# Kernel optimization log

Measured on AMD Instinct MI355X. Metric: run time of the kernel, lower is better.

## Reference

```python
import jax, jax.numpy as jnp
import numpy as np

N = 100_000      # nodes
E = 1_600_000    # directed edges (avg degree 16)
DIN, DH, DOUT = 128, 256, 40
BN_EPS = 1e-5


def setup_inputs() -> dict:
    key = jax.random.key(0)
    ks = jax.random.split(key, 8)
    x = jax.random.normal(ks[0], (N, DIN), jnp.float32)
    edge_index = jax.random.randint(ks[1], (2, E), 0, N, dtype=jnp.int64)
    W0 = jax.random.normal(ks[2], (DIN, DH), jnp.float32) / np.float32(np.sqrt(DIN))
    b0 = jnp.zeros((DH,), jnp.float32)
    Wh = jax.random.normal(ks[3], (3, DH, DH), jnp.float32) / np.float32(np.sqrt(DH))
    bh = jnp.zeros((3, DH), jnp.float32)
    gamma = jnp.ones((4, DH), jnp.float32)
    beta = jnp.zeros((4, DH), jnp.float32)
    Wl = jax.random.normal(ks[4], (DH, DOUT), jnp.float32) / np.float32(np.sqrt(DH))
    bl = jnp.zeros((DOUT,), jnp.float32)
    return dict(x=x, W0=W0, b0=b0, Wh=Wh, bh=bh, gamma=gamma, beta=beta,
                Wl=Wl, bl=bl, edge_index=edge_index)


def _gcn_conv(x, W, b, row, col, norm):
    # x: [N, Din] -> [N, Dout]; GCNConv: D^-1/2 (A+I) D^-1/2 (X W) + b
    h = x @ W
    msg = h[col] * norm[:, None]          # gather over edges [E+N, Dout]
    agg = jax.ops.segment_sum(msg, row, num_segments=N)
    return agg + b


def _bn(x, g, b):
    # BatchNorm1d training-mode math: batch stats over nodes, biased variance
    mu = x.mean(axis=0)
    var = x.var(axis=0)
    return (x - mu) * jax.lax.rsqrt(var + BN_EPS) * g + b


def reference(x, W0, b0, Wh, bh, gamma, beta, Wl, bl, edge_index):
    loop = jnp.arange(N, dtype=edge_index.dtype)
    row = jnp.concatenate([edge_index[0], loop])   # add self-loops
    col = jnp.concatenate([edge_index[1], loop])
    deg = jax.ops.segment_sum(jnp.ones_like(row, x.dtype), row, num_segments=N)
    dinv = jnp.where(deg > 0, jax.lax.rsqrt(jnp.maximum(deg, 1e-12)), 0.0)
    norm = dinv[row] * dinv[col]

    h = _gcn_conv(x, W0, b0, row, col, norm)
    h = jax.nn.relu(_bn(h, gamma[0], beta[0]))
    for i in range(3):
        h = _gcn_conv(h, Wh[i], bh[i], row, col, norm)
        h = jax.nn.relu(_bn(h, gamma[i + 1], beta[i + 1]))
    h = _gcn_conv(h, Wl, bl, row, col, norm)
    return jax.nn.log_softmax(h, axis=-1)
```

## Files before the change

kernel.cpp:

```cpp
#include <hip/hip_runtime.h>
#include <hip/hip_bf16.h>
#include <math.h>
#include <stdint.h>

#define N_NODES 100000
#define N_EDGES 1600000
#define DIN 128
#define DH 256
#define DOUT 40
#define DOUTP 48
#define BN_EPS 1e-5f
#define SCAN_BLOCKS ((N_NODES + 1023) / 1024)

#define RPB 512
#define NBKT ((N_NODES + RPB - 1) / RPB)
#define BCAP 10240
#define EPB 8192

#define AGG_GRID 2048

typedef __attribute__((ext_vector_type(8))) short short8;
typedef __attribute__((ext_vector_type(4))) short short4v;
typedef __attribute__((ext_vector_type(4))) float floatx4;

__device__ __forceinline__ short f2bf(float f) {
    uint32_t u = __float_as_uint(f);
    uint32_t r = u + 0x7FFF + ((u >> 16) & 1);
    return (short)(r >> 16);
}
__device__ __forceinline__ float bf_lo(uint32_t u) { return __uint_as_float(u << 16); }
__device__ __forceinline__ float bf_hi(uint32_t u) { return __uint_as_float(u & 0xFFFF0000u); }
__device__ __forceinline__ float bfval(short s) {
    return __uint_as_float(((uint32_t)(unsigned short)s) << 16);
}


__global__ __launch_bounds__(256) void k_bucket(
    const int* __restrict__ row, const int* __restrict__ col,
    int* __restrict__ cnt, int* __restrict__ bcnt, int2* __restrict__ bkt) {
    __shared__ int lcnt[NBKT];
    __shared__ int gbase[NBKT];
    __shared__ unsigned short parr[EPB];
    const int t = threadIdx.x;
    const int e0 = blockIdx.x * EPB;
    for (int i = t; i < NBKT; i += 256) lcnt[i] = 0;
    __syncthreads();
    for (int i = t; i < EPB; i += 256) {
        int e = e0 + i;
        if (e < N_EDGES) {
            int r = row[e];
            atomicAdd(&cnt[r], 1);
            int b = r >> 9;
            parr[i] = (unsigned short)atomicAdd(&lcnt[b], 1);
        }
    }
    __syncthreads();
    for (int i = t; i < NBKT; i += 256)
        gbase[i] = atomicAdd(&bcnt[i], lcnt[i]);
    __syncthreads();
    for (int i = t; i < EPB; i += 256) {
        int e = e0 + i;
        if (e < N_EDGES) {
            int r = row[e];
            int c = col[e];
            int b = r >> 9;
            int pos = gbase[b] + (int)parr[i];
            if (pos < BCAP) bkt[(size_t)b * BCAP + pos] = make_int2(r, c);
        }
    }
}

__global__ __launch_bounds__(256) void k_scan_a(const int* __restrict__ cnt,
                                                int* __restrict__ rowptr,
                                                int* __restrict__ partials,
                                                float* __restrict__ dinv, int n) {
    int t = threadIdx.x;
    int idx = blockIdx.x * 1024 + t * 4;
    int a0 = 0, a1 = 0, a2 = 0, a3 = 0;
    if (idx + 3 < n) {
        int4 v = *(const int4*)(cnt + idx);
        a0 = v.x + 1; a1 = v.y + 1; a2 = v.z + 1; a3 = v.w + 1;
    } else {
        if (idx + 0 < n) a0 = cnt[idx + 0] + 1;
        if (idx + 1 < n) a1 = cnt[idx + 1] + 1;
        if (idx + 2 < n) a2 = cnt[idx + 2] + 1;
        if (idx + 3 < n) a3 = cnt[idx + 3] + 1;
    }
    if (idx + 0 < n) dinv[idx + 0] = rsqrtf((float)a0);
    if (idx + 1 < n) dinv[idx + 1] = rsqrtf((float)a1);
    if (idx + 2 < n) dinv[idx + 2] = rsqrtf((float)a2);
    if (idx + 3 < n) dinv[idx + 3] = rsqrtf((float)a3);
    int tsum = a0 + a1 + a2 + a3;
    int lane = t & 63, wid = t >> 6;
    int incl = tsum;
#pragma unroll
    for (int off = 1; off < 64; off <<= 1) {
        int x = __shfl_up(incl, off);
        if (lane >= off) incl += x;
    }
    __shared__ int wsum[4];
    if (lane == 63) wsum[wid] = incl;
    __syncthreads();
    int woff = 0;
    for (int i = 0; i < wid; i++) woff += wsum[i];
    int excl = woff + incl - tsum;
    if (idx + 0 < n) rowptr[idx + 0] = excl;
    if (idx + 1 < n) rowptr[idx + 1] = excl + a0;
    if (idx + 2 < n) rowptr[idx + 2] = excl + a0 + a1;
    if (idx + 3 < n) rowptr[idx + 3] = excl + a0 + a1 + a2;
    if (t == 255) partials[blockIdx.x] = woff + incl;
}

__global__ __launch_bounds__(128) void k_scan_b(int* __restrict__ partials,
                                                int* __restrict__ rowptr,
                                                int nb, int n) {
    int t = threadIdx.x;
    int v = (t < nb) ? partials[t] : 0;
    int lane = t & 63, wid = t >> 6;
    int incl = v;
#pragma unroll
    for (int off = 1; off < 64; off <<= 1) {
        int x = __shfl_up(incl, off);
        if (lane >= off) incl += x;
    }
    __shared__ int ws[2];
    if (lane == 63) ws[wid] = incl;
    __syncthreads();
    int woff = (wid == 1) ? ws[0] : 0;
    int excl = woff + incl - v;
    if (t < nb) partials[t] = excl;
    if (t == nb - 1) rowptr[n] = excl + v;
}

__global__ __launch_bounds__(256) void k_scan_c(int* __restrict__ rowptr,
                                                const int* __restrict__ partials, int n) {
    int off = partials[blockIdx.x];
    if (off == 0) return;
    int idx = blockIdx.x * 1024 + threadIdx.x * 4;
    if (idx + 3 < n) {
        int4 v = *(const int4*)(rowptr + idx);
        v.x += off; v.y += off; v.z += off; v.w += off;
        *(int4*)(rowptr + idx) = v;
    } else {
        for (int i = 0; i < 4; i++)
            if (idx + i < n) rowptr[idx + i] += off;
    }
}

__global__ __launch_bounds__(256) void k_fillcsr(
    const int* __restrict__ bcnt, const int2* __restrict__ bkt,
    const int* __restrict__ rowptr, int* __restrict__ colidx) {
    __shared__ int lfill[RPB];
    const int b = blockIdx.x, t = threadIdx.x;
    const int base_row = b * RPB;
    for (int i = t; i < RPB; i += 256) lfill[i] = 0;
    __syncthreads();
    int n = bcnt[b]; if (n > BCAP) n = BCAP;
    const int2* bp = bkt + (size_t)b * BCAP;
    for (int i = t; i < n; i += 256) {
        int2 rc = bp[i];
        int p = atomicAdd(&lfill[rc.x - base_row], 1);
        colidx[rowptr[rc.x] + p] = rc.y;
    }
    __syncthreads();
    for (int i = t; i < RPB; i += 256) {
        int r = base_row + i;
        if (r < N_NODES) colidx[rowptr[r + 1] - 1] = r;
    }
}


__global__ void k_prep_all(const float* __restrict__ W0, const float* __restrict__ Wh,
                           const float* __restrict__ Wl, short* __restrict__ wt0,
                           short* __restrict__ wth, short* __restrict__ wtl) {
    int idx = blockIdx.x * blockDim.x + threadIdx.x;
    if (idx < DH * DIN) {
        int n = idx / DIN, k = idx - n * DIN;
        wt0[idx] = f2bf(W0[(size_t)k * DH + n]);
        return;
    }
    idx -= DH * DIN;
    if (idx < 3 * DH * DH) {
        int m = idx / (DH * DH);
        int r = idx - m * (DH * DH);
        int n = r / DH, k = r - n * DH;
        wth[idx] = f2bf(Wh[(size_t)m * DH * DH + (size_t)k * DH + n]);
        return;
    }
    idx -= 3 * DH * DH;
    if (idx < DOUTP * DH) {
        int n = idx / DH, k = idx - n * DH;
        wtl[idx] = (n < DOUT) ? f2bf(Wl[(size_t)k * DOUT + n]) : (short)0;
    }
}


#define BM 64
#define BN_T 256
#define BK 64
#define BKP 72

template <bool ABF16, bool BN_ACT>
__global__ __launch_bounds__(256) void k_gemm_mfma(
    const void* __restrict__ Ap, const short* __restrict__ Wt,
    short* __restrict__ Chs, const float* __restrict__ dinv,
    const float* __restrict__ scale, const float* __restrict__ shift,
    int M, int K) {
    __shared__ __align__(16) short Als[BM * BKP];
    __shared__ __align__(16) short Bls[BN_T * BKP];
    const int t = threadIdx.x;
    const int bm = blockIdx.x * BM;
    const int w = t >> 6, lane = t & 63;
    const int wm = w & 1, wn = w >> 1;
    const int l15 = lane & 15, quad = lane >> 4;

    floatx4 acc[2][8] = {};

    for (int k0 = 0; k0 < K; k0 += BK) {
        {
            int r = t >> 2;
            int c = t & 3;
            int gr = bm + r; if (gr >= M) gr = M - 1;
            short* lp = Als + r * BKP + c * 16;
            if (ABF16) {
                const short* ap = (const short*)Ap + (size_t)gr * K + k0 + c * 16;
                short8 s0 = *(const short8*)(ap);
                short8 s1 = *(const short8*)(ap + 8);
                if (BN_ACT) {
#pragma unroll
                    for (int i = 0; i < 2; i++) {
                        float4 sc = *(const float4*)(scale + k0 + c * 16 + i * 8);
                        float4 sc2 = *(const float4*)(scale + k0 + c * 16 + i * 8 + 4);
                        float4 sh = *(const float4*)(shift + k0 + c * 16 + i * 8);
                        float4 sh2 = *(const float4*)(shift + k0 + c * 16 + i * 8 + 4);
                        short8& s = i ? s1 : s0;
                        short8 o;
                        o[0] = f2bf(fmaxf(fmaf(bfval(s[0]), sc.x, sh.x), 0.f));
                        o[1] = f2bf(fmaxf(fmaf(bfval(s[1]), sc.y, sh.y), 0.f));
                        o[2] = f2bf(fmaxf(fmaf(bfval(s[2]), sc.z, sh.z), 0.f));
                        o[3] = f2bf(fmaxf(fmaf(bfval(s[3]), sc.w, sh.w), 0.f));
                        o[4] = f2bf(fmaxf(fmaf(bfval(s[4]), sc2.x, sh2.x), 0.f));
                        o[5] = f2bf(fmaxf(fmaf(bfval(s[5]), sc2.y, sh2.y), 0.f));
                        o[6] = f2bf(fmaxf(fmaf(bfval(s[6]), sc2.z, sh2.z), 0.f));
                        o[7] = f2bf(fmaxf(fmaf(bfval(s[7]), sc2.w, sh2.w), 0.f));
                        *(short8*)(lp + i * 8) = o;
                    }
                } else {
                    *(short8*)(lp) = s0;
                    *(short8*)(lp + 8) = s1;
                }
            } else {
                const float* ap = (const float*)Ap + (size_t)gr * K + k0 + c * 16;
#pragma unroll
                for (int i = 0; i < 4; i++) {
                    float4 v = *(const float4*)(ap + i * 4);
                    short4v s;
                    s.x = f2bf(v.x); s.y = f2bf(v.y); s.z = f2bf(v.z); s.w = f2bf(v.w);
                    *(short4v*)(lp + i * 4) = s;
                }
            }
        }
        {
            int r0 = t >> 2;
            int c = t & 3;
#pragma unroll
            for (int p = 0; p < 4; p++) {
                int r = r0 + p * 64;
                const short* bp = Wt + (size_t)r * K + k0 + c * 16;
                short* lp = Bls + r * BKP + c * 16;
                *(short8*)(lp) = *(const short8*)(bp);
                *(short8*)(lp + 8) = *(const short8*)(bp + 8);
            }
        }
        __syncthreads();
#pragma unroll
        for (int kc = 0; kc < 2; kc++) {
            short8 af[2], bfr[8];
#pragma unroll
            for (int mi = 0; mi < 2; mi++)
                af[mi] = *(const short8*)(Als + (wm * 32 + mi * 16 + l15) * BKP + kc * 32 + quad * 8);
#pragma unroll
            for (int ni = 0; ni < 8; ni++)
                bfr[ni] = *(const short8*)(Bls + (wn * 128 + ni * 16 + l15) * BKP + kc * 32 + quad * 8);
#pragma unroll
            for (int mi = 0; mi < 2; mi++)
#pragma unroll
                for (int ni = 0; ni < 8; ni++)
                    acc[mi][ni] = __builtin_amdgcn_mfma_f32_16x16x32_bf16(
                        af[mi], bfr[ni], acc[mi][ni], 0, 0, 0);
        }
        __syncthreads();
    }

#pragma unroll
    for (int mi = 0; mi < 2; mi++) {
#pragma unroll
        for (int r = 0; r < 4; r++) {
            int m = bm + wm * 32 + mi * 16 + quad * 4 + r;
            if (m < M) {
                float d = dinv[m];
                size_t base = (size_t)m * BN_T + wn * 128 + l15;
#pragma unroll
                for (int ni = 0; ni < 8; ni++)
                    Chs[base + ni * 16] = f2bf(acc[mi][ni][r] * d);
            }
        }
    }
}


__global__ __launch_bounds__(256) void k_gemm_last(
    const short* __restrict__ A, const short* __restrict__ Wt,
    short* __restrict__ C, const float* __restrict__ dinv,
    const float* __restrict__ scale, const float* __restrict__ shift, int M) {
    __shared__ __align__(16) short Als[BM * BKP];
    __shared__ __align__(16) short Bls[DOUTP * BKP];
    const int t = threadIdx.x;
    const int bm = blockIdx.x * BM;
    const int w = t >> 6, lane = t & 63;
    const int l15 = lane & 15, quad = lane >> 4;
    const int K = DH;

    floatx4 acc[3] = {};

    for (int k0 = 0; k0 < K; k0 += BK) {
        {
            int r = t >> 2;
            int c = t & 3;
            int gr = bm + r; if (gr >= M) gr = M - 1;
            const short* ap = A + (size_t)gr * K + k0 + c * 16;
            short* lp = Als + r * BKP + c * 16;
            short8 s0 = *(const short8*)(ap);
            short8 s1 = *(const short8*)(ap + 8);
#pragma unroll
            for (int i = 0; i < 2; i++) {
                float4 sc = *(const float4*)(scale + k0 + c * 16 + i * 8);
                float4 sc2 = *(const float4*)(scale + k0 + c * 16 + i * 8 + 4);
                float4 sh = *(const float4*)(shift + k0 + c * 16 + i * 8);
                float4 sh2 = *(const float4*)(shift + k0 + c * 16 + i * 8 + 4);
                short8& s = i ? s1 : s0;
                short8 o;
                o[0] = f2bf(fmaxf(fmaf(bfval(s[0]), sc.x, sh.x), 0.f));
                o[1] = f2bf(fmaxf(fmaf(bfval(s[1]), sc.y, sh.y), 0.f));
                o[2] = f2bf(fmaxf(fmaf(bfval(s[2]), sc.z, sh.z), 0.f));
                o[3] = f2bf(fmaxf(fmaf(bfval(s[3]), sc.w, sh.w), 0.f));
                o[4] = f2bf(fmaxf(fmaf(bfval(s[4]), sc2.x, sh2.x), 0.f));
                o[5] = f2bf(fmaxf(fmaf(bfval(s[5]), sc2.y, sh2.y), 0.f));
                o[6] = f2bf(fmaxf(fmaf(bfval(s[6]), sc2.z, sh2.z), 0.f));
                o[7] = f2bf(fmaxf(fmaf(bfval(s[7]), sc2.w, sh2.w), 0.f));
                *(short8*)(lp + i * 8) = o;
            }
        }
        if (t < 192) {
            int r = t >> 2;
            int c = t & 3;
            const short* bp = Wt + (size_t)r * K + k0 + c * 16;
            short* lp = Bls + r * BKP + c * 16;
            *(short8*)(lp) = *(const short8*)(bp);
            *(short8*)(lp + 8) = *(const short8*)(bp + 8);
        }
        __syncthreads();
#pragma unroll
        for (int kc = 0; kc < 2; kc++) {
            short8 af = *(const short8*)(Als + (w * 16 + l15) * BKP + kc * 32 + quad * 8);
#pragma unroll
            for (int ni = 0; ni < 3; ni++) {
                short8 bfr = *(const short8*)(Bls + (ni * 16 + l15) * BKP + kc * 32 + quad * 8);
                acc[ni] = __builtin_amdgcn_mfma_f32_16x16x32_bf16(af, bfr, acc[ni], 0, 0, 0);
            }
        }
        __syncthreads();
    }

#pragma unroll
    for (int r = 0; r < 4; r++) {
        int m = bm + w * 16 + quad * 4 + r;
        if (m >= M) continue;
        float d = dinv[m];
#pragma unroll
        for (int ni = 0; ni < 3; ni++)
            C[(size_t)m * DOUTP + ni * 16 + l15] = f2bf(acc[ni][r] * d);
    }
}


__global__ __launch_bounds__(256) void k_aggregate_bf16(
    const short* __restrict__ hs, const int* __restrict__ rowptr,
    const int* __restrict__ colidx, const float* __restrict__ dinv,
    short* __restrict__ out, float* __restrict__ psum, float* __restrict__ psq) {
    __shared__ float lps[4][DH];
    __shared__ float lpq[4][DH];
    const int w = threadIdx.x >> 6;
    const int lane = threadIdx.x & 63;
    const int half = lane >> 5;
    const int hl = lane & 31;
    const short* base = hs + hl * 8;

    float stat_s[8] = {};
    float stat_q[8] = {};

    for (int node = blockIdx.x * 4 + w; node < N_NODES; node += AGG_GRID * 4) {
        int s = rowptr[node], e = rowptr[node + 1];
        float acc[4][8] = {};
        int i = s + half;
        for (; i + 6 < e; i += 8) {
            int n0 = colidx[i], n1 = colidx[i + 2], n2 = colidx[i + 4], n3 = colidx[i + 6];
            uint4 u0 = *(const uint4*)(base + (size_t)n0 * DH);
            uint4 u1 = *(const uint4*)(base + (size_t)n1 * DH);
            uint4 u2 = *(const uint4*)(base + (size_t)n2 * DH);
            uint4 u3 = *(const uint4*)(base + (size_t)n3 * DH);
            acc[0][0] += bf_lo(u0.x); acc[0][1] += bf_hi(u0.x);
            acc[0][2] += bf_lo(u0.y); acc[0][3] += bf_hi(u0.y);
            acc[0][4] += bf_lo(u0.z); acc[0][5] += bf_hi(u0.z);
            acc[0][6] += bf_lo(u0.w); acc[0][7] += bf_hi(u0.w);
            acc[1][0] += bf_lo(u1.x); acc[1][1] += bf_hi(u1.x);
            acc[1][2] += bf_lo(u1.y); acc[1][3] += bf_hi(u1.y);
            acc[1][4] += bf_lo(u1.z); acc[1][5] += bf_hi(u1.z);
            acc[1][6] += bf_lo(u1.w); acc[1][7] += bf_hi(u1.w);
            acc[2][0] += bf_lo(u2.x); acc[2][1] += bf_hi(u2.x);
            acc[2][2] += bf_lo(u2.y); acc[2][3] += bf_hi(u2.y);
            acc[2][4] += bf_lo(u2.z); acc[2][5] += bf_hi(u2.z);
            acc[2][6] += bf_lo(u2.w); acc[2][7] += bf_hi(u2.w);
            acc[3][0] += bf_lo(u3.x); acc[3][1] += bf_hi(u3.x);
            acc[3][2] += bf_lo(u3.y); acc[3][3] += bf_hi(u3.y);
            acc[3][4] += bf_lo(u3.z); acc[3][5] += bf_hi(u3.z);
            acc[3][6] += bf_lo(u3.w); acc[3][7] += bf_hi(u3.w);
        }
        for (; i < e; i += 2) {
            int n = colidx[i];
            uint4 u = *(const uint4*)(base + (size_t)n * DH);
            acc[0][0] += bf_lo(u.x); acc[0][1] += bf_hi(u.x);
            acc[0][2] += bf_lo(u.y); acc[0][3] += bf_hi(u.y);
            acc[0][4] += bf_lo(u.z); acc[0][5] += bf_hi(u.z);
            acc[0][6] += bf_lo(u.w); acc[0][7] += bf_hi(u.w);
        }
        float d = dinv[node];
        float f[8];
#pragma unroll
        for (int j = 0; j < 8; j++) {
            f[j] = (acc[0][j] + acc[1][j]) + (acc[2][j] + acc[3][j]);
            f[j] += __shfl_xor(f[j], 32);
            f[j] *= d;
        }
        if (half == 0) {
            short8 r;
#pragma unroll
            for (int j = 0; j < 8; j++) {
                r[j] = f2bf(f[j]);
                stat_s[j] += f[j];
                stat_q[j] = fmaf(f[j], f[j], stat_q[j]);
            }
            *(short8*)(out + (size_t)node * DH + hl * 8) = r;
        }
    }

    if (half == 0) {
#pragma unroll
        for (int j = 0; j < 8; j++) {
            lps[w][hl * 8 + j] = stat_s[j];
            lpq[w][hl * 8 + j] = stat_q[j];
        }
    }
    __syncthreads();
    int c = threadIdx.x;
    float S = (lps[0][c] + lps[1][c]) + (lps[2][c] + lps[3][c]);
    float Q = (lpq[0][c] + lpq[1][c]) + (lpq[2][c] + lpq[3][c]);
    atomicAdd(&psum[c], S);
    atomicAdd(&psq[c], Q);
}


__global__ void k_bnfinal(const float* __restrict__ psum, const float* __restrict__ psq,
                          const float* __restrict__ gamma, const float* __restrict__ beta,
                          float* __restrict__ scale, float* __restrict__ shift) {
    int c = threadIdx.x;
    float mu = psum[c] / (float)N_NODES;
    float var = psq[c] / (float)N_NODES - mu * mu;
    float rs = rsqrtf(var + BN_EPS);
    float sc = gamma[c] * rs;
    scale[c] = sc;
    shift[c] = beta[c] - mu * sc;
}


__global__ __launch_bounds__(256) void k_agg_softmax(
    const short* __restrict__ hsl, const int* __restrict__ rowptr,
    const int* __restrict__ colidx, const float* __restrict__ dinv,
    const float* __restrict__ bias, float* __restrict__ out) {
    int gid = blockIdx.x * blockDim.x + threadIdx.x;
    int node = gid >> 6;
    int lane = threadIdx.x & 63;
    if (node >= N_NODES) return;
    int s = rowptr[node], e = rowptr[node + 1];
    float a[8] = {};
    if (lane < DOUTP) {
        const short* base = hsl + lane;
        int i = s;
        for (; i + 8 <= e; i += 8) {
#pragma unroll
            for (int j = 0; j < 8; j++)
                a[j] += bfval(base[(size_t)colidx[i + j] * DOUTP]);
        }
        for (; i < e; i++) a[0] += bfval(base[(size_t)colidx[i] * DOUTP]);
        a[0] = ((a[0] + a[1]) + (a[2] + a[3])) + ((a[4] + a[5]) + (a[6] + a[7]));
    }
    float acc = 0.f;
    if (lane < DOUT) acc = fmaf(a[0], dinv[node], bias[lane]);
    float v = (lane < DOUT) ? acc : -INFINITY;
    float m = v;
#pragma unroll
    for (int off = 32; off; off >>= 1) m = fmaxf(m, __shfl_xor(m, off));
    float ex = (lane < DOUT) ? expf(acc - m) : 0.f;
    float sum = ex;
#pragma unroll
    for (int off = 32; off; off >>= 1) sum += __shfl_xor(sum, off);
    if (lane < DOUT) out[(size_t)node * DOUT + lane] = acc - m - logf(sum);
}


static inline size_t align_up(size_t x, size_t a) { return (x + a - 1) & ~(a - 1); }

extern "C" void kernel_launch(void* const* d_in, const int* in_sizes, int n_in,
                              void* d_out, int out_size, void* d_ws, size_t ws_size,
                              hipStream_t stream) {
    const float* x     = (const float*)d_in[0];
    const float* W0    = (const float*)d_in[1];
    const float* Wh    = (const float*)d_in[3];
    const float* gamma = (const float*)d_in[5];
    const float* beta  = (const float*)d_in[6];
    const float* Wl    = (const float*)d_in[7];
    const float* bl    = (const float*)d_in[8];
    const int* ei      = (const int*)d_in[9];
    const int* row = ei;
    const int* col = ei + N_EDGES;
    float* out = (float*)d_out;

    char* ws = (char*)d_ws;
    size_t off = 0;
    short* h    = (short*)(ws + off); off = align_up(off + (size_t)N_NODES * DH * 2, 256);
    short* hs   = (short*)(ws + off); off = align_up(off + (size_t)N_NODES * DH * 2, 256);
    short* hsl  = (short*)(ws + off); off = align_up(off + (size_t)N_NODES * DOUTP * 2, 256);
    short* wt0  = (short*)(ws + off); off = align_up(off + (size_t)DH * DIN * 2, 256);
    short* wth  = (short*)(ws + off); off = align_up(off + (size_t)3 * DH * DH * 2, 256);
    short* wtl  = (short*)(ws + off); off = align_up(off + (size_t)DOUTP * DH * 2, 256);
    int* colidx = (int*)(ws + off);  off = align_up(off + (size_t)(N_EDGES + N_NODES) * 4, 256);
    int2* bkt   = (int2*)(ws + off); off = align_up(off + (size_t)NBKT * BCAP * 8, 256);
    int* rowptr = (int*)(ws + off);  off = align_up(off + (size_t)(N_NODES + 1) * 4, 256);
    int* partials = (int*)(ws + off); off = align_up(off + (size_t)SCAN_BLOCKS * 4, 256);
    float* dinv = (float*)(ws + off); off = align_up(off + (size_t)N_NODES * 4, 256);
    float* scale = (float*)(ws + off); off = align_up(off + DH * 4, 256);
    float* shift = (float*)(ws + off); off = align_up(off + DH * 4, 256);
    size_t zero_begin = off;
    int* cnt    = (int*)(ws + off);  off = align_up(off + (size_t)N_NODES * 4, 256);
    int* bcnt   = (int*)(ws + off);  off = align_up(off + (size_t)NBKT * 4, 256);
    float* psum = (float*)(ws + off); off = align_up(off + (size_t)4 * DH * 4, 256);
    float* psq  = (float*)(ws + off); off = align_up(off + (size_t)4 * DH * 4, 256);
    size_t zero_end = off;
    (void)ws_size; (void)n_in; (void)in_sizes; (void)out_size;

    hipMemsetAsync(ws + zero_begin, 0, zero_end - zero_begin, stream);

    const int BKT_BLOCKS = (N_EDGES + EPB - 1) / EPB;
    k_bucket<<<BKT_BLOCKS, 256, 0, stream>>>(row, col, cnt, bcnt, bkt);
    k_scan_a<<<SCAN_BLOCKS, 256, 0, stream>>>(cnt, rowptr, partials, dinv, N_NODES);
    k_scan_b<<<1, 128, 0, stream>>>(partials, rowptr, SCAN_BLOCKS, N_NODES);
    k_scan_c<<<SCAN_BLOCKS, 256, 0, stream>>>(rowptr, partials, N_NODES);
    k_fillcsr<<<NBKT, 256, 0, stream>>>(bcnt, bkt, rowptr, colidx);

    const int PREP_N = DH * DIN + 3 * DH * DH + DOUTP * DH;
    k_prep_all<<<(PREP_N + 255) / 256, 256, 0, stream>>>(W0, Wh, Wl, wt0, wth, wtl);

    const int gemm_blocks = (N_NODES + BM - 1) / BM;
    const int agg_blocks = (N_NODES * 64 + 255) / 256;

    k_gemm_mfma<false, false><<<gemm_blocks, 256, 0, stream>>>(
        x, wt0, hs, dinv, nullptr, nullptr, N_NODES, DIN);
    k_aggregate_bf16<<<AGG_GRID, 256, 0, stream>>>(hs, rowptr, colidx, dinv, h,
                                                   psum, psq);
    k_bnfinal<<<1, 256, 0, stream>>>(psum, psq, gamma, beta, scale, shift);

    for (int i = 0; i < 3; i++) {
        k_gemm_mfma<true, true><<<gemm_blocks, 256, 0, stream>>>(
            h, wth + (size_t)i * DH * DH, hs, dinv, scale, shift, N_NODES, DH);
        k_aggregate_bf16<<<AGG_GRID, 256, 0, stream>>>(hs, rowptr, colidx, dinv, h,
                                                       psum + (i + 1) * DH,
                                                       psq + (i + 1) * DH);
        k_bnfinal<<<1, 256, 0, stream>>>(psum + (i + 1) * DH, psq + (i + 1) * DH,
                                         gamma + (size_t)(i + 1) * DH,
                                         beta + (size_t)(i + 1) * DH, scale, shift);
    }

    k_gemm_last<<<gemm_blocks, 256, 0, stream>>>(h, wtl, hsl, dinv, scale, shift, N_NODES);
    k_agg_softmax<<<agg_blocks, 256, 0, stream>>>(hsl, rowptr, colidx, dinv, bl, out);
}
```

Baseline: 1.135 ms.

## Split BatchNorm statistics out of aggregation into a separate reduction kernel

Result: no change. 1.136 ms (+0.1%).

```diff
diff --git a/kernel.cpp b/kernel.cpp
--- a/kernel.cpp
+++ b/kernel.cpp
@@ -17,7 +17,7 @@
 #define BCAP 10240
 #define EPB 8192
 
-#define AGG_GRID 2048
+#define STATS_GRID 1024
 
 typedef __attribute__((ext_vector_type(8))) short short8;
 typedef __attribute__((ext_vector_type(4))) short short4v;
@@ -387,86 +387,95 @@
 __global__ __launch_bounds__(256) void k_aggregate_bf16(
     const short* __restrict__ hs, const int* __restrict__ rowptr,
     const int* __restrict__ colidx, const float* __restrict__ dinv,
-    short* __restrict__ out, float* __restrict__ psum, float* __restrict__ psq) {
-    __shared__ float lps[4][DH];
-    __shared__ float lpq[4][DH];
-    const int w = threadIdx.x >> 6;
-    const int lane = threadIdx.x & 63;
-    const int half = lane >> 5;
-    const int hl = lane & 31;
+    short* __restrict__ out) {
+    int gid = blockIdx.x * blockDim.x + threadIdx.x;
+    int node = gid >> 6;
+    if (node >= N_NODES) return;
+    int lane = threadIdx.x & 63;
+    int half = lane >> 5;
+    int hl = lane & 31;
+    int s = rowptr[node], e = rowptr[node + 1];
     const short* base = hs + hl * 8;
 
-    float stat_s[8] = {};
-    float stat_q[8] = {};
-
-    for (int node = blockIdx.x * 4 + w; node < N_NODES; node += AGG_GRID * 4) {
-        int s = rowptr[node], e = rowptr[node + 1];
-        float acc[4][8] = {};
-        int i = s + half;
-        for (; i + 6 < e; i += 8) {
-            int n0 = colidx[i], n1 = colidx[i + 2], n2 = colidx[i + 4], n3 = colidx[i + 6];
-            uint4 u0 = *(const uint4*)(base + (size_t)n0 * DH);
-            uint4 u1 = *(const uint4*)(base + (size_t)n1 * DH);
-            uint4 u2 = *(const uint4*)(base + (size_t)n2 * DH);
-            uint4 u3 = *(const uint4*)(base + (size_t)n3 * DH);
-            acc[0][0] += bf_lo(u0.x); acc[0][1] += bf_hi(u0.x);
-            acc[0][2] += bf_lo(u0.y); acc[0][3] += bf_hi(u0.y);
-            acc[0][4] += bf_lo(u0.z); acc[0][5] += bf_hi(u0.z);
-            acc[0][6] += bf_lo(u0.w); acc[0][7] += bf_hi(u0.w);
-            acc[1][0] += bf_lo(u1.x); acc[1][1] += bf_hi(u1.x);
-            acc[1][2] += bf_lo(u1.y); acc[1][3] += bf_hi(u1.y);
-            acc[1][4] += bf_lo(u1.z); acc[1][5] += bf_hi(u1.z);
-            acc[1][6] += bf_lo(u1.w); acc[1][7] += bf_hi(u1.w);
-            acc[2][0] += bf_lo(u2.x); acc[2][1] += bf_hi(u2.x);
-            acc[2][2] += bf_lo(u2.y); acc[2][3] += bf_hi(u2.y);
-            acc[2][4] += bf_lo(u2.z); acc[2][5] += bf_hi(u2.z);
-            acc[2][6] += bf_lo(u2.w); acc[2][7] += bf_hi(u2.w);
-            acc[3][0] += bf_lo(u3.x); acc[3][1] += bf_hi(u3.x);
-            acc[3][2] += bf_lo(u3.y); acc[3][3] += bf_hi(u3.y);
-            acc[3][4] += bf_lo(u3.z); acc[3][5] += bf_hi(u3.z);
-            acc[3][6] += bf_lo(u3.w); acc[3][7] += bf_hi(u3.w);
-        }
-        for (; i < e; i += 2) {
-            int n = colidx[i];
-            uint4 u = *(const uint4*)(base + (size_t)n * DH);
-            acc[0][0] += bf_lo(u.x); acc[0][1] += bf_hi(u.x);
-            acc[0][2] += bf_lo(u.y); acc[0][3] += bf_hi(u.y);
-            acc[0][4] += bf_lo(u.z); acc[0][5] += bf_hi(u.z);
-            acc[0][6] += bf_lo(u.w); acc[0][7] += bf_hi(u.w);
-        }
+    float acc[4][8] = {};
+    int i = s + half;
+    for (; i + 6 < e; i += 8) {
+        int n0 = colidx[i], n1 = colidx[i + 2], n2 = colidx[i + 4], n3 = colidx[i + 6];
+        uint4 u0 = *(const uint4*)(base + (size_t)n0 * DH);
+        uint4 u1 = *(const uint4*)(base + (size_t)n1 * DH);
+        uint4 u2 = *(const uint4*)(base + (size_t)n2 * DH);
+        uint4 u3 = *(const uint4*)(base + (size_t)n3 * DH);
+        acc[0][0] += bf_lo(u0.x); acc[0][1] += bf_hi(u0.x);
+        acc[0][2] += bf_lo(u0.y); acc[0][3] += bf_hi(u0.y);
+        acc[0][4] += bf_lo(u0.z); acc[0][5] += bf_hi(u0.z);
+        acc[0][6] += bf_lo(u0.w); acc[0][7] += bf_hi(u0.w);
+        acc[1][0] += bf_lo(u1.x); acc[1][1] += bf_hi(u1.x);
+        acc[1][2] += bf_lo(u1.y); acc[1][3] += bf_hi(u1.y);
+        acc[1][4] += bf_lo(u1.z); acc[1][5] += bf_hi(u1.z);
+        acc[1][6] += bf_lo(u1.w); acc[1][7] += bf_hi(u1.w);
+        acc[2][0] += bf_lo(u2.x); acc[2][1] += bf_hi(u2.x);
+        acc[2][2] += bf_lo(u2.y); acc[2][3] += bf_hi(u2.y);
+        acc[2][4] += bf_lo(u2.z); acc[2][5] += bf_hi(u2.z);
+        acc[2][6] += bf_lo(u2.w); acc[2][7] += bf_hi(u2.w);
+        acc[3][0] += bf_lo(u3.x); acc[3][1] += bf_hi(u3.x);
+        acc[3][2] += bf_lo(u3.y); acc[3][3] += bf_hi(u3.y);
+        acc[3][4] += bf_lo(u3.z); acc[3][5] += bf_hi(u3.z);
+        acc[3][6] += bf_lo(u3.w); acc[3][7] += bf_hi(u3.w);
+    }
+    for (; i < e; i += 2) {
+        int n = colidx[i];
+        uint4 u = *(const uint4*)(base + (size_t)n * DH);
+        acc[0][0] += bf_lo(u.x); acc[0][1] += bf_hi(u.x);
+        acc[0][2] += bf_lo(u.y); acc[0][3] += bf_hi(u.y);
+        acc[0][4] += bf_lo(u.z); acc[0][5] += bf_hi(u.z);
+        acc[0][6] += bf_lo(u.w); acc[0][7] += bf_hi(u.w);
+    }
+    float f[8];
+#pragma unroll
+    for (int j = 0; j < 8; j++) {
+        f[j] = (acc[0][j] + acc[1][j]) + (acc[2][j] + acc[3][j]);
+        f[j] += __shfl_xor(f[j], 32);
+    }
+    if (half == 0) {
         float d = dinv[node];
-        float f[8];
+        short8 r;
+#pragma unroll
+        for (int j = 0; j < 8; j++) r[j] = f2bf(f[j] * d);
+        *(short8*)(out + (size_t)node * DH + hl * 8) = r;
+    }
+}
+
+
+__global__ __launch_bounds__(256) void k_bnstats(const short* __restrict__ h,
+                                                 float* __restrict__ psum,
+                                                 float* __restrict__ psq) {
+    __shared__ float lps[DH];
+    __shared__ float lpq[DH];
+    const int t = threadIdx.x;
+    const int cg = t & 31;
+    const int ro = t >> 5;
+    if (t < DH) { lps[t] = 0.f; lpq[t] = 0.f; }
+    __syncthreads();
+    float s[8] = {}, q[8] = {};
+    for (int r = blockIdx.x * 8 + ro; r < N_NODES; r += STATS_GRID * 8) {
+        short8 v = *(const short8*)(h + (size_t)r * DH + cg * 8);
 #pragma unroll
         for (int j = 0; j < 8; j++) {
-            f[j] = (acc[0][j] + acc[1][j]) + (acc[2][j] + acc[3][j]);
-            f[j] += __shfl_xor(f[j], 32);
-            f[j] *= d;
-        }
-        if (half == 0) {
-            short8 r;
-#pragma unroll
-            for (int j = 0; j < 8; j++) {
-                r[j] = f2bf(f[j]);
-                stat_s[j] += f[j];
-                stat_q[j] = fmaf(f[j], f[j], stat_q[j]);
-            }
-            *(short8*)(out + (size_t)node * DH + hl * 8) = r;
-        }
-    }
-
-    if (half == 0) {
-#pragma unroll
-        for (int j = 0; j < 8; j++) {
-            lps[w][hl * 8 + j] = stat_s[j];
-            lpq[w][hl * 8 + j] = stat_q[j];
-        }
-    }
-    __syncthreads();
-    int c = threadIdx.x;
-    float S = (lps[0][c] + lps[1][c]) + (lps[2][c] + lps[3][c]);
-    float Q = (lpq[0][c] + lpq[1][c]) + (lpq[2][c] + lpq[3][c]);
-    atomicAdd(&psum[c], S);
-    atomicAdd(&psq[c], Q);
+            float f = bfval(v[j]);
+            s[j] += f;
+            q[j] = fmaf(f, f, q[j]);
+        }
+    }
+#pragma unroll
+    for (int j = 0; j < 8; j++) {
+        atomicAdd(&lps[cg * 8 + j], s[j]);
+        atomicAdd(&lpq[cg * 8 + j], q[j]);
+    }
+    __syncthreads();
+    if (t < DH) {
+        atomicAdd(&psum[t], lps[t]);
+        atomicAdd(&psq[t], lpq[t]);
+    }
 }
 
 
@@ -575,16 +584,16 @@
 
     k_gemm_mfma<false, false><<<gemm_blocks, 256, 0, stream>>>(
         x, wt0, hs, dinv, nullptr, nullptr, N_NODES, DIN);
-    k_aggregate_bf16<<<AGG_GRID, 256, 0, stream>>>(hs, rowptr, colidx, dinv, h,
-                                                   psum, psq);
+    k_aggregate_bf16<<<agg_blocks, 256, 0, stream>>>(hs, rowptr, colidx, dinv, h);
+    k_bnstats<<<STATS_GRID, 256, 0, stream>>>(h, psum, psq);
     k_bnfinal<<<1, 256, 0, stream>>>(psum, psq, gamma, beta, scale, shift);
 
     for (int i = 0; i < 3; i++) {
         k_gemm_mfma<true, true><<<gemm_blocks, 256, 0, stream>>>(
             h, wth + (size_t)i * DH * DH, hs, dinv, scale, shift, N_NODES, DH);
-        k_aggregate_bf16<<<AGG_GRID, 256, 0, stream>>>(hs, rowptr, colidx, dinv, h,
-                                                       psum + (i + 1) * DH,
-                                                       psq + (i + 1) * DH);
+        k_aggregate_bf16<<<agg_blocks, 256, 0, stream>>>(hs, rowptr, colidx, dinv, h);
+        k_bnstats<<<STATS_GRID, 256, 0, stream>>>(h, psum + (i + 1) * DH,
+                                                  psq + (i + 1) * DH);
         k_bnfinal<<<1, 256, 0, stream>>>(psum + (i + 1) * DH, psq + (i + 1) * DH,
                                          gamma + (size_t)(i + 1) * DH,
                                          beta + (size_t)(i + 1) * DH, scale, shift);
```
